# Kernel tuning notes

Hardware: AMD Instinct MI355X
Metric: run time of the kernel (lower is better)

## Reference

```python
import jax, jax.numpy as jnp
import numpy as np

B, S, D = 2, 2048, 1024
H, HKV = 16, 4
HD = D // H          # 64
NREP = H // HKV      # 4
EPS = 1e-6
ROPE_BASE = 10000.0


def setup_inputs() -> dict:
    key = jax.random.key(0)
    ks = jax.random.split(key, 6)
    std = 0.02
    return {
        "x": jax.random.normal(ks[0], (B, S, D), dtype=jnp.float32),
        "Wq": jax.random.normal(ks[1], (D, H * HD), dtype=jnp.float32) * std,
        "Wk": jax.random.normal(ks[2], (D, HKV * HD), dtype=jnp.float32) * std,
        "Wv": jax.random.normal(ks[3], (D, HKV * HD), dtype=jnp.float32) * std,
        "Wo": jax.random.normal(ks[4], (D, D), dtype=jnp.float32) * std,
        "norm_w": jnp.ones((D,), dtype=jnp.float32),
    }


def _rope_cos_sin(seq_len, head_dim, dtype):
    inv_freq = 1.0 / (ROPE_BASE ** (jnp.arange(0, head_dim, 2, dtype=jnp.float32) / head_dim))
    t = jnp.arange(seq_len, dtype=jnp.float32)
    freqs = jnp.outer(t, inv_freq)                 # [S, HD/2]
    emb = jnp.concatenate([freqs, freqs], axis=-1)  # [S, HD]
    return jnp.cos(emb).astype(dtype), jnp.sin(emb).astype(dtype)


def _rotate_half(x):
    x1, x2 = jnp.split(x, 2, axis=-1)
    return jnp.concatenate([-x2, x1], axis=-1)


def _apply_rope(x, cos, sin):
    # x: [B, nh, S, HD]; cos/sin: [S, HD]
    return x * cos[None, None] + _rotate_half(x) * sin[None, None]


def reference(x, Wq, Wk, Wv, Wo, norm_w):
    b, s, _ = x.shape
    q = (x @ Wq).reshape(b, s, H, HD).transpose(0, 2, 1, 3)      # [B,H,S,HD]
    k = (x @ Wk).reshape(b, s, HKV, HD).transpose(0, 2, 1, 3)    # [B,HKV,S,HD]
    v = (x @ Wv).reshape(b, s, HKV, HD).transpose(0, 2, 1, 3)

    cos, sin = _rope_cos_sin(s, HD, x.dtype)
    q = _apply_rope(q, cos, sin)
    k = _apply_rope(k, cos, sin)

    # repeat kv heads to match q heads
    k = jnp.repeat(k, NREP, axis=1)   # [B,H,S,HD]
    v = jnp.repeat(v, NREP, axis=1)

    scale = HD ** -0.5
    scores = jnp.einsum('bhqd,bhkd->bhqk', q, k) * scale   # [B,H,S,S]
    attn = jax.nn.softmax(scores, axis=-1)
    out = jnp.einsum('bhqk,bhkd->bhqd', attn, v)            # [B,H,S,HD]
    out = out.transpose(0, 2, 1, 3).reshape(b, s, D)
    out = out @ Wo

    # RMSNorm
    rms = jnp.sqrt(jnp.mean(out * out, axis=-1, keepdims=True) + EPS)
    out = out / rms * norm_w
    return out
```

## Files before the change

### kernel.cpp

```cpp
#include <hip/hip_runtime.h>
#include <hip/hip_bf16.h>
#include <stdint.h>
#include <math.h>

typedef __bf16 bf16x8 __attribute__((ext_vector_type(8)));
typedef float f32x4 __attribute__((ext_vector_type(4)));
typedef float f32x16 __attribute__((ext_vector_type(16)));

#define B_    2
#define S_    2048
#define D_    1024
#define H_    16
#define HKV_  4
#define HD_   64
#define MTOT  4096
#define NQKV  1536
#define BHS   65536

#define ZERO16 {0.f,0.f,0.f,0.f,0.f,0.f,0.f,0.f,0.f,0.f,0.f,0.f,0.f,0.f,0.f,0.f}

__device__ __forceinline__ unsigned short f2bf(float f) {
  union { float f; unsigned u; } v; v.f = f;
  unsigned r = (v.u + 0x7FFFu + ((v.u >> 16) & 1u)) >> 16;
  return (unsigned short)r;
}

__device__ __forceinline__ float bf2f(unsigned short u) {
  union { unsigned u; float f; } v; v.u = (unsigned)u << 16; return v.f;
}

__device__ __forceinline__ float fast_exp2(float x) {
  return __builtin_amdgcn_exp2f(x);
}

__device__ __forceinline__ unsigned cvt_pk_bf16(float lo, float hi) {
  unsigned r;
  asm("v_cvt_pk_bf16_f32 %0, %1, %2" : "=v"(r) : "v"(lo), "v"(hi));
  return r;
}

__device__ __forceinline__ void gl_lds16(const void* g, void* l) {
  __builtin_amdgcn_global_load_lds((const __attribute__((address_space(1))) void*)g,
                                   (__attribute__((address_space(3))) void*)l, 16, 0, 0);
}

__global__ __launch_bounds__(256) void k_pre(const float* __restrict__ Wq, const float* __restrict__ Wk,
                                             const float* __restrict__ Wv, const float* __restrict__ Wo,
                                             const float* __restrict__ x,
                                             unsigned short* __restrict__ wqkvt,
                                             unsigned short* __restrict__ wot,
                                             unsigned short* __restrict__ xb,
                                             float* __restrict__ cost, float* __restrict__ sint) {
  int bid = blockIdx.x, tid = threadIdx.x;
  if (bid < 640) {
    const float* src; unsigned short* dst; int ldsrc, cb, rb;
    if (bid < 256)      { src = Wq; dst = wqkvt;                          ldsrc = 1024; cb = (bid & 15) * 64; rb = (bid >> 4) * 64; }
    else if (bid < 320) { int i = bid - 256; src = Wk; dst = wqkvt + (size_t)1024 * 1024; ldsrc = 256; cb = (i & 3) * 64; rb = (i >> 2) * 64; }
    else if (bid < 384) { int i = bid - 320; src = Wv; dst = wqkvt + (size_t)1280 * 1024; ldsrc = 256; cb = (i & 3) * 64; rb = (i >> 2) * 64; }
    else                { int i = bid - 384; src = Wo; dst = wot;         ldsrc = 1024; cb = (i & 15) * 64; rb = (i >> 4) * 64; }
    __shared__ unsigned short T[64][72];
    for (int rep = 0; rep < 4; ++rep) {
      int idx = rep * 256 + tid;
      int r = idx >> 4, seg = idx & 15;
      float4 v = *(const float4*)&src[(size_t)(rb + r) * ldsrc + cb + seg * 4];
      T[seg*4+0][r] = f2bf(v.x);
      T[seg*4+1][r] = f2bf(v.y);
      T[seg*4+2][r] = f2bf(v.z);
      T[seg*4+3][r] = f2bf(v.w);
    }
    __syncthreads();
    for (int rep = 0; rep < 2; ++rep) {
      int idx = rep * 256 + tid;
      int c = idx >> 3, seg = idx & 7;
      *(uint4*)&dst[(size_t)(cb + c) * 1024 + rb + seg * 8] = *(const uint4*)&T[c][seg * 8];
    }
  } else if (bid < 896) {
    int idx = (bid - 640) * 256 + tid;
    int s = idx >> 5, i = idx & 31;
    double inv = exp(-(double)i / 32.0 * log(10000.0));
    double ang = (double)s * inv;
    cost[idx] = (float)cos(ang);
    sint[idx] = (float)sin(ang);
  } else {
    int i = (bid - 896) * 256 + tid;
    const int n4 = MTOT * D_ / 4;
    for (; i < n4; i += 1024 * 256) {
      float4 v = ((const float4*)x)[i];
      ushort4 o;
      o.x = f2bf(v.x); o.y = f2bf(v.y); o.z = f2bf(v.z); o.w = f2bf(v.w);
      ((ushort4*)xb)[i] = o;
    }
  }
}

__global__ __launch_bounds__(256) void k_gemm_qkv(const unsigned short* __restrict__ A,
                                                  const unsigned short* __restrict__ Bt,
                                                  const float* __restrict__ cost,
                                                  const float* __restrict__ sint,
                                                  unsigned short* __restrict__ Qb,
                                                  unsigned short* __restrict__ Kb,
                                                  unsigned short* __restrict__ Vt) {
  int nb = blockIdx.x, mb = blockIdx.y;
  __shared__ unsigned short Arena[2][12288];
  int tid = threadIdx.x, lane = tid & 63, w = tid >> 6;
  int wr = w >> 1, wc = w & 1;
  f32x4 acc[2][4];
  for (int m = 0; m < 2; ++m) for (int n = 0; n < 4; ++n) acc[m][n] = (f32x4){0.f, 0.f, 0.f, 0.f};

  const int rl = lane >> 3;
  const int csw = ((lane & 7) ^ rl) * 8;

  auto stage = [&](int buf, int kt) {
    for (int j = 0; j < 2; ++j)
      gl_lds16(&A[(size_t)(mb * 64 + w * 16 + j * 8 + rl) * D_ + kt * 64 + csw],
               &Arena[buf][(w * 16 + j * 8) * 64]);
    for (int j = 0; j < 4; ++j)
      gl_lds16(&Bt[(size_t)(nb * 128 + w * 32 + j * 8 + rl) * D_ + kt * 64 + csw],
               &Arena[buf][4096 + (w * 32 + j * 8) * 64]);
  };
  stage(0, 0);
  const int NT = D_ / 64;
  int cur = 0;
  const int lr = lane & 15, lg = lane >> 4, swl = lane & 7;
  for (int kt = 0; kt < NT; ++kt) {
    __syncthreads();
    if (kt + 1 < NT) stage(cur ^ 1, kt + 1);
    #pragma unroll
    for (int kk = 0; kk < 2; ++kk) {
      int ch = ((kk * 4 + lg) ^ swl) * 8;
      bf16x8 af[2], bfr[4];
      for (int m = 0; m < 2; ++m) af[m]  = *(const bf16x8*)&Arena[cur][(wr * 32 + m * 16 + lr) * 64 + ch];
      for (int n = 0; n < 4; ++n) bfr[n] = *(const bf16x8*)&Arena[cur][4096 + (wc * 64 + n * 16 + lr) * 64 + ch];
      for (int m = 0; m < 2; ++m)
        for (int n = 0; n < 4; ++n)
          acc[m][n] = __builtin_amdgcn_mfma_f32_16x16x32_bf16(af[m], bfr[n], acc[m][n], 0, 0, 0);
    }
    cur ^= 1;
  }

  const int lq = (lane >> 4) * 4;
  const int b = mb >> 5;
  const int s0 = (mb & 31) * 64;

  if (nb < 10) {
    const float QSCALE = 0.18033688011112042f;
    float scl = (nb < 8) ? QSCALE : 1.f;
    #pragma unroll
    for (int m = 0; m < 2; ++m) {
      #pragma unroll
      for (int n = 0; n < 4; ++n) {
        int gc = nb * 128 + wc * 64 + n * 16 + lr;
        int d  = gc & 63, d2 = d & 31;
        float sgn = (d < 32) ? -1.f : 1.f;
        unsigned short* dst;
        if (nb < 8) {
          int h = gc >> 6;
          dst = Qb + (((size_t)(b * H_ + h)) * S_) * HD_ + d;
        } else {
          int hk = (gc - 1024) >> 6;
          dst = Kb + (((size_t)(b * HKV_ + hk)) * S_) * HD_ + d;
        }
        #pragma unroll
        for (int r = 0; r < 4; ++r) {
          int s = s0 + wr * 32 + m * 16 + lq + r;
          float c  = cost[s * 32 + d2];
          float sn = sint[s * 32 + d2];
          float xv = acc[m][n][r];
          float xp = acc[m][n ^ 2][r];
          float o = (xv * c + sgn * xp * sn) * scl;
          dst[(size_t)s * HD_] = f2bf(o);
        }
      }
    }
  } else {
    __syncthreads();
    unsigned short* T = &Arena[0][0];
    #pragma unroll
    for (int m = 0; m < 2; ++m)
      #pragma unroll
      for (int n = 0; n < 4; ++n)
        #pragma unroll
        for (int r = 0; r < 4; ++r) {
          int c = wc * 64 + n * 16 + lr;
          int rw = wr * 32 + m * 16 + lq + r;
          T[c * 72 + rw] = f2bf(acc[m][n][r]);
        }
    __syncthreads();
    {
      int j = tid >> 1, q = tid & 1;
      int v_off = (nb - 10) * 128 + j;
      int hk = v_off >> 6, dl = v_off & 63;
      unsigned short* dst = Vt + (((size_t)(b * HKV_ + hk)) * HD_ + dl) * S_ + s0 + q * 32;
      const unsigned short* srcp = &T[j * 72 + q * 32];
      #pragma unroll
      for (int k2 = 0; k2 < 4; ++k2)
        *(uint4*)&dst[k2 * 8] = *(const uint4*)&srcp[k2 * 8];
    }
  }
}

__global__ __launch_bounds__(256) void k_gemm_bt(const unsigned short* __restrict__ A,
                                                 const unsigned short* __restrict__ Bt,
                                                 unsigned short* __restrict__ C0,
                                                 unsigned short* __restrict__ C1,
                                                 int M, int N, int Kfull) {
  int nb = blockIdx.x, mb = blockIdx.y, z = blockIdx.z;
  int kbase = z * (Kfull >> 1);
  int Klen = Kfull >> 1;
  unsigned short* C = z ? C1 : C0;
  __shared__ unsigned short Arena[2][12288];
  int tid = threadIdx.x, lane = tid & 63, w = tid >> 6;
  int wr = w >> 1, wc = w & 1;
  f32x4 acc[2][4];
  for (int m = 0; m < 2; ++m) for (int n = 0; n < 4; ++n) acc[m][n] = (f32x4){0.f, 0.f, 0.f, 0.f};

  const int rl = lane >> 3;
  const int csw = ((lane & 7) ^ rl) * 8;

  auto stage = [&](int buf, int kt) {
    for (int j = 0; j < 2; ++j)
      gl_lds16(&A[(size_t)(mb * 64 + w * 16 + j * 8 + rl) * Kfull + kbase + kt * 64 + csw],
               &Arena[buf][(w * 16 + j * 8) * 64]);
    for (int j = 0; j < 4; ++j)
      gl_lds16(&Bt[(size_t)(nb * 128 + w * 32 + j * 8 + rl) * Kfull + kbase + kt * 64 + csw],
               &Arena[buf][4096 + (w * 32 + j * 8) * 64]);
  };
  stage(0, 0);
  int NT = Klen / 64;
  int cur = 0;
  const int lr = lane & 15, lg = lane >> 4, swl = lane & 7;
  for (int kt = 0; kt < NT; ++kt) {
    __syncthreads();
    if (kt + 1 < NT) stage(cur ^ 1, kt + 1);
    #pragma unroll
    for (int kk = 0; kk < 2; ++kk) {
      int ch = ((kk * 4 + lg) ^ swl) * 8;
      bf16x8 af[2], bfr[4];
      for (int m = 0; m < 2; ++m) af[m]  = *(const bf16x8*)&Arena[cur][(wr * 32 + m * 16 + lr) * 64 + ch];
      for (int n = 0; n < 4; ++n) bfr[n] = *(const bf16x8*)&Arena[cur][4096 + (wc * 64 + n * 16 + lr) * 64 + ch];
      for (int m = 0; m < 2; ++m)
        for (int n = 0; n < 4; ++n)
          acc[m][n] = __builtin_amdgcn_mfma_f32_16x16x32_bf16(af[m], bfr[n], acc[m][n], 0, 0, 0);
    }
    cur ^= 1;
  }
  int lq = (lane >> 4) * 4;
  for (int m = 0; m < 2; ++m)
    for (int n = 0; n < 4; ++n)
      for (int r = 0; r < 4; ++r)
        C[(size_t)(mb * 64 + wr * 32 + m * 16 + lq + r) * N + nb * 128 + wc * 64 + n * 16 + lr] =
            f2bf(acc[m][n][r]);
}

__global__ __launch_bounds__(512, 2) void k_attn(const unsigned short* __restrict__ Q,
                                                 const unsigned short* __restrict__ K,
                                                 const unsigned short* __restrict__ Vt,
                                                 unsigned short* __restrict__ Ob) {
  int wg = ((blockIdx.x & 7) << 6) | (blockIdx.x >> 3);
  int qt = wg & 15;
  int bh = wg >> 4;
  int b = bh >> 4, h = bh & 15, hk = h >> 2;
  const unsigned short* Qp = Q + (((size_t)(b * H_ + h)) * S_ + qt * 128) * HD_;
  const unsigned short* Kp = K + ((size_t)(b * HKV_ + hk)) * S_ * HD_;
  const unsigned short* Vp = Vt + ((size_t)(b * HKV_ + hk)) * HD_ * S_;

  __shared__ unsigned short Lds[2 * 16384];

  const int tid = threadIdx.x, lane = tid & 63, w = tid >> 6;
  const int g  = w >> 2;
  const int wl = w & 3;
  const int col = lane & 31;
  const int hi  = lane >> 5;
  const int sw  = lane & 7;
  const int kv0 = g * (S_ / 2);
  const int gbase = g * 16384;

  const unsigned short* pka[4];
  #pragma unroll
  for (int kc = 0; kc < 4; ++kc)
    pka[kc] = &Lds[gbase + col * 64 + ((kc * 2 + hi) ^ sw) * 8];

  bf16x8 qf[4];
  {
    const unsigned short* qrow = Qp + (size_t)(wl * 32 + col) * HD_;
    #pragma unroll
    for (int dc = 0; dc < 4; ++dc)
      qf[dc] = *(const bf16x8*)&qrow[dc * 16 + hi * 8];
  }

  union { unsigned short s[8]; bf16x8 v; } onesu;
  #pragma unroll
  for (int i = 0; i < 8; ++i) onesu.s[i] = 0x3F80;
  const bf16x8 ones = onesu.v;

  f32x16 oacc0 = ZERO16, oacc1 = ZERO16, lacc = ZERO16;

  const int rl = lane >> 3, cs = lane & 7;
  const int row0 = wl * 16 + rl;
  const int csrc = (cs ^ (row0 & 7)) * 8;
  const unsigned short* srcK = &Kp[(size_t)(kv0 + row0) * HD_ + csrc];
  const unsigned short* srcV = &Vp[(size_t)row0 * S_ + kv0 + csrc];

  auto stage = [&](int be) {
    gl_lds16(srcK,           &Lds[gbase + be + (wl * 16) * 64]);
    gl_lds16(srcK + 8 * HD_, &Lds[gbase + be + (wl * 16 + 8) * 64]);
    gl_lds16(srcV,           &Lds[gbase + be + 8192 + (wl * 16) * 64]);
    gl_lds16(srcV + 8 * S_,  &Lds[gbase + be + 8192 + (wl * 16 + 8) * 64]);
    srcK += 64 * HD_;
    srcV += 64;
  };

  auto compute = [&](int be) {
    bf16x8 pf[4];
    #pragma unroll
    for (int blk2 = 0; blk2 < 2; ++blk2) {
      f32x16 st = ZERO16;
      __builtin_amdgcn_s_setprio(1);
      #pragma unroll
      for (int kc = 0; kc < 4; ++kc) {
        bf16x8 kf = *(const bf16x8*)(pka[kc] + be + blk2 * 2048);
        st = __builtin_amdgcn_mfma_f32_32x32x16_bf16(kf, qf[kc], st, 0, 0, 0);
      }
      __builtin_amdgcn_s_setprio(0);
      #pragma unroll
      for (int i = 0; i < 16; ++i)
        st[i] = fast_exp2(st[i]);
      #pragma unroll
      for (int kcl = 0; kcl < 2; ++kcl) {
        int base = kcl * 8;
        unsigned u0 = cvt_pk_bf16(st[base + 0], st[base + 1]);
        unsigned u1 = cvt_pk_bf16(st[base + 2], st[base + 3]);
        unsigned u2 = cvt_pk_bf16(st[base + 4], st[base + 5]);
        unsigned u3 = cvt_pk_bf16(st[base + 6], st[base + 7]);
        asm("v_permlane32_swap_b32 %0, %1" : "+v"(u0), "+v"(u2));
        asm("v_permlane32_swap_b32 %0, %1" : "+v"(u1), "+v"(u3));
        union { unsigned u[4]; bf16x8 v; } pk;
        pk.u[0] = u0; pk.u[1] = u1; pk.u[2] = u2; pk.u[3] = u3;
        pf[blk2 * 2 + kcl] = pk.v;
      }
    }
    __builtin_amdgcn_s_setprio(1);
    #pragma unroll
    for (int kc = 0; kc < 4; ++kc)
      lacc = __builtin_amdgcn_mfma_f32_32x32x16_bf16(ones, pf[kc], lacc, 0, 0, 0);
    #pragma unroll
    for (int kc = 0; kc < 4; ++kc) {
      bf16x8 v0 = *(const bf16x8*)(pka[kc] + be + 8192);
      bf16x8 v1 = *(const bf16x8*)(pka[kc] + be + 8192 + 2048);
      oacc0 = __builtin_amdgcn_mfma_f32_32x32x16_bf16(v0, pf[kc], oacc0, 0, 0, 0);
      oacc1 = __builtin_amdgcn_mfma_f32_32x32x16_bf16(v1, pf[kc], oacc1, 0, 0, 0);
    }
    __builtin_amdgcn_s_setprio(0);
  };

  stage(0);
  for (int it = 0; it < 8; ++it) {
    __syncthreads();
    stage(4096);
    compute(0);
    __syncthreads();
    if (it < 7) stage(0);
    compute(4096);
  }

  __syncthreads();
  float* xch = (float*)Lds;
  if (g == 0) {
    float* slot = xch + ((size_t)wl * 64 + lane) * 33;
    #pragma unroll
    for (int i = 0; i < 16; ++i) { slot[i] = oacc0[i]; slot[16 + i] = oacc1[i]; }
    slot[32] = lacc[0];
  }
  __syncthreads();
  if (g == 1) {
    const float* slot = xch + ((size_t)wl * 64 + lane) * 33;
    float rinv = 1.f / (lacc[0] + slot[32]);
    int qrow = qt * 128 + wl * 32 + col;
    unsigned short* ob = Ob + ((size_t)(b * S_ + qrow)) * D_ + h * 64;
    #pragma unroll
    for (int rr = 0; rr < 4; ++rr) {
      ushort4 o0, o1;
      o0.x = f2bf((oacc0[rr*4+0] + slot[rr*4+0]) * rinv);
      o0.y = f2bf((oacc0[rr*4+1] + slot[rr*4+1]) * rinv);
      o0.z = f2bf((oacc0[rr*4+2] + slot[rr*4+2]) * rinv);
      o0.w = f2bf((oacc0[rr*4+3] + slot[rr*4+3]) * rinv);
      o1.x = f2bf((oacc1[rr*4+0] + slot[16+rr*4+0]) * rinv);
      o1.y = f2bf((oacc1[rr*4+1] + slot[16+rr*4+1]) * rinv);
      o1.z = f2bf((oacc1[rr*4+2] + slot[16+rr*4+2]) * rinv);
      o1.w = f2bf((oacc1[rr*4+3] + slot[16+rr*4+3]) * rinv);
      *(ushort4*)&ob[8 * rr + 4 * hi]      = o0;
      *(ushort4*)&ob[32 + 8 * rr + 4 * hi] = o1;
    }
  }
}

__global__ __launch_bounds__(256) void k_rmsnorm(const unsigned short* __restrict__ in0,
                                                 const unsigned short* __restrict__ in1,
                                                 const float* __restrict__ wt,
                                                 float* __restrict__ out) {
  int row = blockIdx.x, tid = threadIdx.x;
  ushort4 u0 = *(const ushort4*)&in0[(size_t)row * D_ + tid * 4];
  ushort4 u1 = *(const ushort4*)&in1[(size_t)row * D_ + tid * 4];
  float x0 = bf2f(u0.x) + bf2f(u1.x);
  float x1 = bf2f(u0.y) + bf2f(u1.y);
  float x2 = bf2f(u0.z) + bf2f(u1.z);
  float x3 = bf2f(u0.w) + bf2f(u1.w);
  float ss = x0 * x0 + x1 * x1 + x2 * x2 + x3 * x3;
  for (int o = 32; o >= 1; o >>= 1) ss += __shfl_xor(ss, o);
  __shared__ float red[4];
  if ((tid & 63) == 0) red[tid >> 6] = ss;
  __syncthreads();
  float tot = red[0] + red[1] + red[2] + red[3];
  float rinv = 1.f / sqrtf(tot * (1.f / 1024.f) + 1e-6f);
  float4 wv = ((const float4*)wt)[tid];
  float4 o;
  o.x = x0 * rinv * wv.x;
  o.y = x1 * rinv * wv.y;
  o.z = x2 * rinv * wv.z;
  o.w = x3 * rinv * wv.w;
  ((float4*)(out + (size_t)row * D_))[tid] = o;
}

extern "C" void kernel_launch(void* const* d_in, const int* in_sizes, int n_in,
                              void* d_out, int out_size, void* d_ws, size_t ws_size,
                              hipStream_t stream) {
  const float* x  = (const float*)d_in[0];
  const float* Wq = (const float*)d_in[1];
  const float* Wk = (const float*)d_in[2];
  const float* Wv = (const float*)d_in[3];
  const float* Wo = (const float*)d_in[4];
  const float* nw = (const float*)d_in[5];
  float* out = (float*)d_out;

  char* p = (char*)d_ws;
  unsigned short* xb    = (unsigned short*)p; p += (size_t)MTOT * D_ * 2;
  char*           slot  = p;                  p += (size_t)18 * 1024 * 1024;
  unsigned short* wqkvt = (unsigned short*)p; p += (size_t)NQKV * D_ * 2;
  unsigned short* wot   = (unsigned short*)p; p += (size_t)D_ * D_ * 2;
  unsigned short* qb    = (unsigned short*)p; p += (size_t)B_ * H_ * S_ * HD_ * 2;
  unsigned short* kb    = (unsigned short*)p; p += (size_t)B_ * HKV_ * S_ * HD_ * 2;
  unsigned short* vtb   = (unsigned short*)p; p += (size_t)B_ * HKV_ * HD_ * S_ * 2;
  char*           big2  = p;                  p += (size_t)MTOT * D_ * 2 * 2;
  float*          mlold = (float*)p;          p += (size_t)2 * BHS * 4;
  float*          cost  = (float*)p;          p += (size_t)S_ * 32 * 4;
  float*          sint  = (float*)p;          p += (size_t)S_ * 32 * 4;
  (void)mlold;

  unsigned short* attnb   = (unsigned short*)big2;
  unsigned short* proj_p0 = (unsigned short*)slot;
  unsigned short* proj_p1 = (unsigned short*)(slot + (size_t)MTOT * D_ * 2);

  k_pre<<<1920, 256, 0, stream>>>(Wq, Wk, Wv, Wo, x, wqkvt, wot, xb, cost, sint);

  k_gemm_qkv<<<dim3(NQKV / 128, MTOT / 64), 256, 0, stream>>>(xb, wqkvt, cost, sint, qb, kb, vtb);
  k_attn<<<512, 512, 0, stream>>>(qb, kb, vtb, attnb);
  k_gemm_bt<<<dim3(D_ / 128, MTOT / 64, 2), 256, 0, stream>>>(attnb, wot, proj_p0, proj_p1, MTOT, D_, D_);
  k_rmsnorm<<<MTOT, 256, 0, stream>>>(proj_p0, proj_p1, nw, out);
}
```

Before: 94.31 us.

## Software-pipeline attention loop: overlap QK of next tile with PV of previous

Restructures the attention inner loop so that the QK matmul for tile T is issued alongside the PV matmul for tile T-1, with exp/pack happening afterward. V gets a triple-buffered LDS ring while K stays double-buffered, which grows LDS per block. Launch bounds are raised to request 4 blocks per CU, which squeezes the register budget. The aim is to hide exp latency and LDS waits behind MFMA work, at the cost of register pressure and possible spilling.

```diff
diff --git a/kernel.cpp b/kernel.cpp
--- a/kernel.cpp
+++ b/kernel.cpp
@@ -252,7 +252,7 @@
             f2bf(acc[m][n][r]);
 }
 
-__global__ __launch_bounds__(512, 2) void k_attn(const unsigned short* __restrict__ Q,
+__global__ __launch_bounds__(512, 4) void k_attn(const unsigned short* __restrict__ Q,
                                                  const unsigned short* __restrict__ K,
                                                  const unsigned short* __restrict__ Vt,
                                                  unsigned short* __restrict__ Ob) {
@@ -264,7 +264,7 @@
   const unsigned short* Kp = K + ((size_t)(b * HKV_ + hk)) * S_ * HD_;
   const unsigned short* Vp = Vt + ((size_t)(b * HKV_ + hk)) * HD_ * S_;
 
-  __shared__ unsigned short Lds[2 * 16384];
+  __shared__ unsigned short Lds[2 * 20480];
 
   const int tid = threadIdx.x, lane = tid & 63, w = tid >> 6;
   const int g  = w >> 2;
@@ -273,7 +273,7 @@
   const int hi  = lane >> 5;
   const int sw  = lane & 7;
   const int kv0 = g * (S_ / 2);
-  const int gbase = g * 16384;
+  const int gbase = g * 20480;
 
   const unsigned short* pka[4];
   #pragma unroll
@@ -294,6 +294,8 @@
   const bf16x8 ones = onesu.v;
 
   f32x16 oacc0 = ZERO16, oacc1 = ZERO16, lacc = ZERO16;
+  f32x16 st0, st1;
+  bf16x8 pf[4];
 
   const int rl = lane >> 3, cs = lane & 7;
   const int row0 = wl * 16 + rl;
@@ -301,67 +303,83 @@
   const unsigned short* srcK = &Kp[(size_t)(kv0 + row0) * HD_ + csrc];
   const unsigned short* srcV = &Vp[(size_t)row0 * S_ + kv0 + csrc];
 
-  auto stage = [&](int be) {
-    gl_lds16(srcK,           &Lds[gbase + be + (wl * 16) * 64]);
-    gl_lds16(srcK + 8 * HD_, &Lds[gbase + be + (wl * 16 + 8) * 64]);
-    gl_lds16(srcV,           &Lds[gbase + be + 8192 + (wl * 16) * 64]);
-    gl_lds16(srcV + 8 * S_,  &Lds[gbase + be + 8192 + (wl * 16 + 8) * 64]);
+  auto stage = [&](int ko, int vo) {
+    gl_lds16(srcK,           &Lds[gbase + ko + (wl * 16) * 64]);
+    gl_lds16(srcK + 8 * HD_, &Lds[gbase + ko + (wl * 16 + 8) * 64]);
+    gl_lds16(srcV,           &Lds[gbase + vo + (wl * 16) * 64]);
+    gl_lds16(srcV + 8 * S_,  &Lds[gbase + vo + (wl * 16 + 8) * 64]);
     srcK += 64 * HD_;
     srcV += 64;
   };
 
-  auto compute = [&](int be) {
-    bf16x8 pf[4];
-    #pragma unroll
-    for (int blk2 = 0; blk2 < 2; ++blk2) {
-      f32x16 st = ZERO16;
-      __builtin_amdgcn_s_setprio(1);
-      #pragma unroll
-      for (int kc = 0; kc < 4; ++kc) {
-        bf16x8 kf = *(const bf16x8*)(pka[kc] + be + blk2 * 2048);
-        st = __builtin_amdgcn_mfma_f32_32x32x16_bf16(kf, qf[kc], st, 0, 0, 0);
-      }
-      __builtin_amdgcn_s_setprio(0);
-      #pragma unroll
-      for (int i = 0; i < 16; ++i)
-        st[i] = fast_exp2(st[i]);
+  auto qk = [&](int ko) {
+    st0 = (f32x16)ZERO16; st1 = (f32x16)ZERO16;
+    __builtin_amdgcn_s_setprio(1);
+    #pragma unroll
+    for (int kc = 0; kc < 4; ++kc) {
+      bf16x8 k0 = *(const bf16x8*)(pka[kc] + ko);
+      bf16x8 k1 = *(const bf16x8*)(pka[kc] + ko + 2048);
+      st0 = __builtin_amdgcn_mfma_f32_32x32x16_bf16(k0, qf[kc], st0, 0, 0, 0);
+      st1 = __builtin_amdgcn_mfma_f32_32x32x16_bf16(k1, qf[kc], st1, 0, 0, 0);
+    }
+    __builtin_amdgcn_s_setprio(0);
+  };
+
+  auto pv = [&](int vo) {
+    __builtin_amdgcn_s_setprio(1);
+    #pragma unroll
+    for (int kc = 0; kc < 4; ++kc) {
+      bf16x8 v0 = *(const bf16x8*)(pka[kc] + vo);
+      bf16x8 v1 = *(const bf16x8*)(pka[kc] + vo + 2048);
+      lacc  = __builtin_amdgcn_mfma_f32_32x32x16_bf16(ones, pf[kc], lacc, 0, 0, 0);
+      oacc0 = __builtin_amdgcn_mfma_f32_32x32x16_bf16(v0, pf[kc], oacc0, 0, 0, 0);
+      oacc1 = __builtin_amdgcn_mfma_f32_32x32x16_bf16(v1, pf[kc], oacc1, 0, 0, 0);
+    }
+    __builtin_amdgcn_s_setprio(0);
+  };
+
+  auto expack = [&]() {
+    #pragma unroll
+    for (int i = 0; i < 16; ++i) { st0[i] = fast_exp2(st0[i]); st1[i] = fast_exp2(st1[i]); }
+    #pragma unroll
+    for (int kb2 = 0; kb2 < 2; ++kb2) {
+      const f32x16& s = kb2 ? st1 : st0;
       #pragma unroll
       for (int kcl = 0; kcl < 2; ++kcl) {
         int base = kcl * 8;
-        unsigned u0 = cvt_pk_bf16(st[base + 0], st[base + 1]);
-        unsigned u1 = cvt_pk_bf16(st[base + 2], st[base + 3]);
-        unsigned u2 = cvt_pk_bf16(st[base + 4], st[base + 5]);
-        unsigned u3 = cvt_pk_bf16(st[base + 6], st[base + 7]);
+        unsigned u0 = cvt_pk_bf16(s[base + 0], s[base + 1]);
+        unsigned u1 = cvt_pk_bf16(s[base + 2], s[base + 3]);
+        unsigned u2 = cvt_pk_bf16(s[base + 4], s[base + 5]);
+        unsigned u3 = cvt_pk_bf16(s[base + 6], s[base + 7]);
         asm("v_permlane32_swap_b32 %0, %1" : "+v"(u0), "+v"(u2));
         asm("v_permlane32_swap_b32 %0, %1" : "+v"(u1), "+v"(u3));
         union { unsigned u[4]; bf16x8 v; } pk;
         pk.u[0] = u0; pk.u[1] = u1; pk.u[2] = u2; pk.u[3] = u3;
-        pf[blk2 * 2 + kcl] = pk.v;
+        pf[kb2 * 2 + kcl] = pk.v;
       }
     }
-    __builtin_amdgcn_s_setprio(1);
-    #pragma unroll
-    for (int kc = 0; kc < 4; ++kc)
-      lacc = __builtin_amdgcn_mfma_f32_32x32x16_bf16(ones, pf[kc], lacc, 0, 0, 0);
-    #pragma unroll
-    for (int kc = 0; kc < 4; ++kc) {
-      bf16x8 v0 = *(const bf16x8*)(pka[kc] + be + 8192);
-      bf16x8 v1 = *(const bf16x8*)(pka[kc] + be + 8192 + 2048);
-      oacc0 = __builtin_amdgcn_mfma_f32_32x32x16_bf16(v0, pf[kc], oacc0, 0, 0, 0);
-      oacc1 = __builtin_amdgcn_mfma_f32_32x32x16_bf16(v1, pf[kc], oacc1, 0, 0, 0);
-    }
-    __builtin_amdgcn_s_setprio(0);
-  };
-
-  stage(0);
-  for (int it = 0; it < 8; ++it) {
-    __syncthreads();
-    stage(4096);
-    compute(0);
-    __syncthreads();
-    if (it < 7) stage(0);
-    compute(4096);
-  }
+  };
+
+#define KO_(T) (((T) & 1) * 4096)
+#define VO_(T) (8192 + ((T) % 3) * 4096)
+#define STEP(T, NOTLAST, NOTFIRST)                                   \
+  do {                                                               \
+    __syncthreads();                                                 \
+    if (NOTLAST) stage(KO_((T) + 1), VO_((T) + 1));                  \
+    qk(KO_(T));                                                      \
+    if (NOTFIRST) pv(VO_((T) - 1));                                  \
+    expack();                                                        \
+  } while (0)
+
+  stage(KO_(0), VO_(0));
+  STEP(0, 1, 0);  STEP(1, 1, 1);  STEP(2, 1, 1);  STEP(3, 1, 1);
+  STEP(4, 1, 1);  STEP(5, 1, 1);  STEP(6, 1, 1);  STEP(7, 1, 1);
+  STEP(8, 1, 1);  STEP(9, 1, 1);  STEP(10, 1, 1); STEP(11, 1, 1);
+  STEP(12, 1, 1); STEP(13, 1, 1); STEP(14, 1, 1); STEP(15, 0, 1);
+  pv(VO_(15));
+#undef STEP
+#undef KO_
+#undef VO_
 
   __syncthreads();
   float* xch = (float*)Lds;
```

After: 103.5 us. +9.8%, slower.
